# Performance work log

Measured on AMD Instinct MI355X. Metric: run time of the kernel, lower is better.

The kernel has to match this reference:

```python
import jax, jax.numpy as jnp
import numpy as np
import math

A, B, C = 32, 2048, 256   # batch, seq_len, features (M_size1)
TK, HA = 3, 8             # num_blocks, num_heads
DH = C // HA
EPS = 1e-5


def _layernorm(x, g, b):
    mu = jnp.mean(x, axis=-1, keepdims=True)
    var = jnp.mean((x - mu) ** 2, axis=-1, keepdims=True)
    return (x - mu) * jax.lax.rsqrt(var + EPS) * g + b


def setup_inputs() -> dict:
    key = jax.random.key(0)
    ks = jax.random.split(key, 12)
    # NOTE: torch code uses randn (std=1) for weight/Wqkv/Wo which explodes
    # numerically over 3 blocks + 2048-step cumsum; we use a small-std init
    # (like the trunc_normal(std=0.02) used for bias/cls) for a well-scaled
    # baseline. The math of the forward pass is unchanged.
    s = 0.02
    return {
        "x": jax.random.normal(ks[0], (A, B, C), jnp.float32),
        "weight": s * jax.random.normal(ks[1], (C, C), jnp.float32),
        "bias": s * jax.random.normal(ks[2], (A, B + 1, C), jnp.float32),
        "cls": s * jax.random.normal(ks[3], (A, 1, C), jnp.float32),
        "Wqkv": s * jax.random.normal(ks[4], (TK, 3, HA, DH, C), jnp.float32),
        "Wo": s * jax.random.normal(ks[5], (TK, C, C), jnp.float32),
        "ln1_g": jnp.ones((C,), jnp.float32),
        "ln1_b": jnp.zeros((C,), jnp.float32),
        "ln2_g": jnp.ones((C,), jnp.float32),
        "ln2_b": jnp.zeros((C,), jnp.float32),
        "fc1_w": s * jax.random.normal(ks[6], (4 * C, C), jnp.float32),
        "fc1_b": jnp.zeros((4 * C,), jnp.float32),
        "fc2_w": s * jax.random.normal(ks[7], (C, 4 * C), jnp.float32),
        "fc2_b": jnp.zeros((C,), jnp.float32),
    }


def reference(x, weight, bias, cls, Wqkv, Wo, ln1_g, ln1_b, ln2_g, ln2_b,
              fc1_w, fc1_b, fc2_w, fc2_b):
    # savespace[i,j,l] = sum_m weight[l,m] * x[i,j,m]   (torch: 'lm,jmi->ijl')
    savespace = jnp.einsum('ijm,lm->ijl', x, weight)              # (A,B,C)
    savespace = jnp.concatenate([cls, savespace], axis=1) + bias  # (A,B+1,C)

    inv_sqrt_dh = 1.0 / math.sqrt(DH)
    for a in range(TK):
        z = _layernorm(savespace, ln1_g, ln1_b)
        # (3,HA,DH,C) x (A,B+1,C) -> (3,A,B+1,HA,DH)
        qkv = jnp.einsum('xhdm,ijm->xijhd', Wqkv[a], z)
        q, k, v = qkv[0], qkv[1], qkv[2]
        rsa = jnp.sum(q * k, axis=-1) * inv_sqrt_dh               # (A,B+1,HA)
        imv = rsa[..., None] * v                                  # (A,B+1,HA,DH)
        # torch loop: subj in range(1, B) -> cumsum over positions 0..B-1,
        # last position (index B) left untouched.
        imv = jnp.concatenate(
            [jnp.cumsum(imv[:, :B], axis=1), imv[:, B:]], axis=1)
        imv = imv.reshape(A, B + 1, C)
        savespace = jnp.einsum('nm,ijm->ijn', Wo[a], imv) + savespace
        z2 = _layernorm(savespace, ln2_g, ln2_b)
        h = jax.nn.gelu(z2 @ fc1_w.T + fc1_b, approximate=False)
        savespace = h @ fc2_w.T + fc2_b + savespace
    return savespace
```

## Files before the change

### kernel.cpp

```cpp
#include <hip/hip_runtime.h>
#include <math.h>

#define AA 32
#define BB 2048
#define BP1 2049
#define CC 256
#define NROWS (AA * BP1)
#define NBLK 3
#define FFN 1024

typedef unsigned int uint;
typedef unsigned short ushort_t;
typedef __attribute__((ext_vector_type(4))) float f32x4;
typedef __attribute__((ext_vector_type(8))) short short8;

#define F_ROWMAP 2
#define F_BIAS2D 4
#define F_BIAS1D 8
#define F_GELU   16
#define F_RESID  32
#define F_OUTB16 64
#define F_QKV    128

__device__ __forceinline__ float bf2f(ushort_t u) {
    return __uint_as_float(((uint)u) << 16);
}
__device__ __forceinline__ ushort_t f2b(float x) {
    uint u = __float_as_uint(x);
    u += 0x7fff + ((u >> 16) & 1);
    return (ushort_t)(u >> 16);
}

typedef const uint __attribute__((address_space(1)))* gas_t;
typedef uint __attribute__((address_space(3)))* las_t;
__device__ __forceinline__ void gload16(const ushort_t* g, const short* l) {
    __builtin_amdgcn_global_load_lds(
        reinterpret_cast<gas_t>(reinterpret_cast<uintptr_t>(g)),
        reinterpret_cast<las_t>(static_cast<uint>(reinterpret_cast<uintptr_t>(l))),
        16, 0, 0);
}

__global__ __launch_bounds__(256) void pack2_k(const float* __restrict__ src,
                                               ushort_t* __restrict__ dh,
                                               ushort_t* __restrict__ dl, int n) {
    int i = blockIdx.x * 256 + threadIdx.x;
    if (i < n) {
        float v = src[i];
        ushort_t h = f2b(v);
        dh[i] = h;
        if (dl) dl[i] = f2b(v - bf2f(h));
    }
}

__global__ __launch_bounds__(256) void wqkv_pack_k(const float* __restrict__ src,
                                                   ushort_t* __restrict__ dh,
                                                   ushort_t* __restrict__ dl) {
    int i = blockIdx.x * 256 + threadIdx.x;
    if (i >= 589824) return;
    int c = i & 255;
    int rr = (i >> 8) % 768;
    int a = i / (768 * 256);
    int srcrow;
    if (rr < 512) {
        int head = rr >> 6, half = (rr >> 5) & 1, d = rr & 31;
        srcrow = half * 256 + head * 32 + d;
    } else {
        srcrow = rr;
    }
    float v = src[((size_t)a * 768 + srcrow) * 256 + c];
    ushort_t h = f2b(v);
    dh[i] = h;
    dl[i] = f2b(v - bf2f(h));
}

__global__ __launch_bounds__(256) void row0_k(float* __restrict__ out,
                                              const float* __restrict__ cls,
                                              const float* __restrict__ bias) {
    int i = blockIdx.x, t = threadIdx.x;
    size_t o = (size_t)i * BP1 * CC + t;
    out[o] = cls[i * CC + t] + bias[o];
}

__global__ __launch_bounds__(256) void ln_k(const float* __restrict__ in,
                                            ushort_t* __restrict__ zh, ushort_t* __restrict__ zl,
                                            const float* __restrict__ g, const float* __restrict__ b) {
    int row = blockIdx.x * 4 + (threadIdx.x >> 6);
    int lane = threadIdx.x & 63;
    const float4 v = *reinterpret_cast<const float4*>(in + (size_t)row * CC + lane * 4);
    float s = v.x + v.y + v.z + v.w;
    float sq = v.x * v.x + v.y * v.y + v.z * v.z + v.w * v.w;
    #pragma unroll
    for (int m = 1; m < 64; m <<= 1) { s += __shfl_xor(s, m); sq += __shfl_xor(sq, m); }
    float mu = s * (1.0f / CC);
    float var = sq * (1.0f / CC) - mu * mu;
    float rs = rsqrtf(var + 1e-5f);
    const float4 gg = *reinterpret_cast<const float4*>(g + lane * 4);
    const float4 bb = *reinterpret_cast<const float4*>(b + lane * 4);
    float o[4];
    o[0] = (v.x - mu) * rs * gg.x + bb.x;
    o[1] = (v.y - mu) * rs * gg.y + bb.y;
    o[2] = (v.z - mu) * rs * gg.z + bb.z;
    o[3] = (v.w - mu) * rs * gg.w + bb.w;
    ushort4 hs;
    hs.x = f2b(o[0]); hs.y = f2b(o[1]); hs.z = f2b(o[2]); hs.w = f2b(o[3]);
    size_t base = (size_t)row * CC + lane * 4;
    *reinterpret_cast<ushort4*>(zh + base) = hs;
    if (zl) {
        ushort4 ls;
        ls.x = f2b(o[0] - bf2f(hs.x));
        ls.y = f2b(o[1] - bf2f(hs.y));
        ls.z = f2b(o[2] - bf2f(hs.z));
        ls.w = f2b(o[3] - bf2f(hs.w));
        *reinterpret_cast<ushort4*>(zl + base) = ls;
    }
}

__global__ __launch_bounds__(256) void cumsum1_k(const ushort_t* __restrict__ v,
                                                 const float* __restrict__ rsa,
                                                 float* __restrict__ tot) {
    int bi = blockIdx.x >> 5, ch = blockIdx.x & 31, c = threadIdx.x;
    int h = c >> 5;
    size_t row0 = (size_t)bi * BP1 + ch * 64;
    float s = 0.f;
    for (int j = 0; j < 64; ++j)
        s += bf2f(v[(row0 + j) * CC + c]) * rsa[(row0 + j) * 8 + h];
    tot[((size_t)bi * 32 + ch) * CC + c] = s;
}

__global__ __launch_bounds__(256) void cumsum2_k(const ushort_t* __restrict__ v,
                                                 const float* __restrict__ rsa,
                                                 const float* __restrict__ tot,
                                                 ushort_t* __restrict__ ph) {
    int bi = blockIdx.x / 33, ch = blockIdx.x - bi * 33, c = threadIdx.x;
    int h = c >> 5;
    if (ch == 32) {
        size_t row = (size_t)bi * BP1 + BB;
        float val = bf2f(v[row * CC + c]) * rsa[row * 8 + h];
        ph[row * CC + c] = f2b(val);
        return;
    }
    float s = 0.f;
    for (int q = 0; q < ch; ++q) s += tot[((size_t)bi * 32 + q) * CC + c];
    size_t row0 = (size_t)bi * BP1 + ch * 64;
    for (int j = 0; j < 64; ++j) {
        size_t row = row0 + j;
        s += bf2f(v[row * CC + c]) * rsa[row * 8 + h];
        ph[row * CC + c] = f2b(s);
    }
}

template<int ALO, int WLO>
__global__ __launch_bounds__(64) void mm_k(const ushort_t* __restrict__ Ah_g,
                                           const ushort_t* __restrict__ Al_g,
                                           const ushort_t* __restrict__ Bh_g,
                                           const ushort_t* __restrict__ Bl_g,
                                           void* __restrict__ Op,
                                           void* __restrict__ Op2,
                                           const float* __restrict__ bias,
                                           int M, int K, int NC, int NT, int flags) {
    __shared__ __align__(16) short As_h[2048];
    __shared__ __align__(16) short As_l[ALO ? 2048 : 8];
    __shared__ __align__(16) short Bs_h[2048];
    __shared__ __align__(16) short Bs_l[WLO ? 2048 : 8];
    const int l = threadIdx.x;

    const int nwg = gridDim.x;
    const int q8 = nwg >> 3, r8 = nwg & 7;
    const int xcd = blockIdx.x & 7, ii = blockIdx.x >> 3;
    const int wgid = (xcd < r8 ? xcd * (q8 + 1) : r8 * (q8 + 1) + (xcd - r8) * q8) + ii;
    const int nt = wgid % NT, mt = wgid / NT;
    const int n0 = nt * 64, m0 = mt * 64;

    const int sc = (l & 3) * 8;
    const int lr = l >> 2;
    size_t aoff[4], boff[4];
    #pragma unroll
    for (int c = 0; c < 4; ++c) {
        int ra = m0 + c * 16 + lr; if (ra >= M) ra = M - 1;
        aoff[c] = (size_t)ra * K + sc;
        boff[c] = (size_t)(n0 + c * 16 + lr) * K + sc;
    }

    f32x4 acc[4][4];
    #pragma unroll
    for (int i = 0; i < 4; ++i)
        #pragma unroll
        for (int j = 0; j < 4; ++j) acc[i][j] = (f32x4)(0.0f);

    for (int k0 = 0; k0 < K; k0 += 32) {
        #pragma unroll
        for (int c = 0; c < 4; ++c) {
            gload16(Ah_g + aoff[c] + k0, &As_h[c * 512]);
            if (ALO) gload16(Al_g + aoff[c] + k0, &As_l[c * 512]);
            gload16(Bh_g + boff[c] + k0, &Bs_h[c * 512]);
            if (WLO) gload16(Bl_g + boff[c] + k0, &Bs_l[c * 512]);
        }
        asm volatile("s_waitcnt vmcnt(0)" ::: "memory");
        __builtin_amdgcn_sched_barrier(0);
        short8 ah[4], al[4], bh[4], bl[4];
        #pragma unroll
        for (int i = 0; i < 4; ++i) {
            int ro = (i * 16 + (l & 15)) * 32 + (l >> 4) * 8;
            ah[i] = *reinterpret_cast<const short8*>(&As_h[ro]);
            if (ALO) al[i] = *reinterpret_cast<const short8*>(&As_l[ro]);
        }
        #pragma unroll
        for (int j = 0; j < 4; ++j) {
            int ro = (j * 16 + (l & 15)) * 32 + (l >> 4) * 8;
            bh[j] = *reinterpret_cast<const short8*>(&Bs_h[ro]);
            if (WLO) bl[j] = *reinterpret_cast<const short8*>(&Bs_l[ro]);
        }
        #pragma unroll
        for (int i = 0; i < 4; ++i)
            #pragma unroll
            for (int j = 0; j < 4; ++j) {
                acc[i][j] = __builtin_amdgcn_mfma_f32_16x16x32_bf16(bh[j], ah[i], acc[i][j], 0, 0, 0);
                if (WLO)
                    acc[i][j] = __builtin_amdgcn_mfma_f32_16x16x32_bf16(bl[j], ah[i], acc[i][j], 0, 0, 0);
                if (ALO)
                    acc[i][j] = __builtin_amdgcn_mfma_f32_16x16x32_bf16(bh[j], al[i], acc[i][j], 0, 0, 0);
            }
        __builtin_amdgcn_sched_barrier(0);
    }

    if (flags & F_QKV) {
        const int cb0 = n0;
        if (cb0 < 512) {
            float* rsaO = reinterpret_cast<float*>(Op);
            const int head = cb0 >> 6;
            #pragma unroll
            for (int i = 0; i < 4; ++i) {
                int row = m0 + i * 16 + (l & 15);
                float p = 0.f;
                #pragma unroll
                for (int j = 0; j < 2; ++j)
                    #pragma unroll
                    for (int r = 0; r < 4; ++r)
                        p += acc[i][j][r] * acc[i][j + 2][r];
                p += __shfl_xor(p, 16);
                p += __shfl_xor(p, 32);
                if (l < 16 && row < M)
                    rsaO[(size_t)row * 8 + head] = p * 0.17677669529663689f;
            }
        } else {
            ushort_t* vO = reinterpret_cast<ushort_t*>(Op2);
            #pragma unroll
            for (int i = 0; i < 4; ++i) {
                int row = m0 + i * 16 + (l & 15);
                if (row >= M) continue;
                #pragma unroll
                for (int j = 0; j < 4; ++j) {
                    int colb = cb0 + j * 16 + (l >> 4) * 4 - 512;
                    uint2 u;
                    u.x = (uint)f2b(acc[i][j][0]) | ((uint)f2b(acc[i][j][1]) << 16);
                    u.y = (uint)f2b(acc[i][j][2]) | ((uint)f2b(acc[i][j][3]) << 16);
                    *reinterpret_cast<uint2*>(vO + (size_t)row * 256 + colb) = u;
                }
            }
        }
        return;
    }

    #pragma unroll
    for (int i = 0; i < 4; ++i) {
        int row = m0 + i * 16 + (l & 15);
        if (row >= M) continue;
        size_t g = (flags & F_ROWMAP) ? ((size_t)(row >> 11) * BP1 + 1 + (row & 2047))
                                     : (size_t)row;
        #pragma unroll
        for (int j = 0; j < 4; ++j) {
            int col0 = n0 + j * 16 + (l >> 4) * 4;
            float4 v4 = make_float4(acc[i][j][0], acc[i][j][1], acc[i][j][2], acc[i][j][3]);
            if (flags & F_BIAS1D) {
                const float4 b4 = *reinterpret_cast<const float4*>(bias + col0);
                v4.x += b4.x; v4.y += b4.y; v4.z += b4.z; v4.w += b4.w;
            }
            if (flags & F_BIAS2D) {
                const float4 b4 = *reinterpret_cast<const float4*>(bias + g * (size_t)NC + col0);
                v4.x += b4.x; v4.y += b4.y; v4.z += b4.z; v4.w += b4.w;
            }
            if (flags & F_GELU) {
                float z0 = v4.x * (1.595769122f + 0.071354816f * v4.x * v4.x);
                float z1 = v4.y * (1.595769122f + 0.071354816f * v4.y * v4.y);
                float z2 = v4.z * (1.595769122f + 0.071354816f * v4.z * v4.z);
                float z3 = v4.w * (1.595769122f + 0.071354816f * v4.w * v4.w);
                v4.x = v4.x / (1.0f + __expf(-z0));
                v4.y = v4.y / (1.0f + __expf(-z1));
                v4.z = v4.z / (1.0f + __expf(-z2));
                v4.w = v4.w / (1.0f + __expf(-z3));
            }
            size_t oi = g * (size_t)NC + col0;
            if (flags & F_OUTB16) {
                uint2 u;
                u.x = (uint)f2b(v4.x) | ((uint)f2b(v4.y) << 16);
                u.y = (uint)f2b(v4.z) | ((uint)f2b(v4.w) << 16);
                *reinterpret_cast<uint2*>(reinterpret_cast<ushort_t*>(Op) + oi) = u;
            } else {
                float* O = reinterpret_cast<float*>(Op) + oi;
                if (flags & F_RESID) {
                    const float4 o4 = *reinterpret_cast<const float4*>(O);
                    v4.x += o4.x; v4.y += o4.y; v4.z += o4.z; v4.w += o4.w;
                }
                *reinterpret_cast<float4*>(O) = v4;
            }
        }
    }
}

extern "C" void kernel_launch(void* const* d_in, const int* in_sizes, int n_in,
                              void* d_out, int out_size, void* d_ws, size_t ws_size,
                              hipStream_t stream) {
    const float* x      = (const float*)d_in[0];
    const float* weight = (const float*)d_in[1];
    const float* bias   = (const float*)d_in[2];
    const float* cls    = (const float*)d_in[3];
    const float* Wqkv   = (const float*)d_in[4];
    const float* Wo     = (const float*)d_in[5];
    const float* ln1_g  = (const float*)d_in[6];
    const float* ln1_b  = (const float*)d_in[7];
    const float* ln2_g  = (const float*)d_in[8];
    const float* ln2_b  = (const float*)d_in[9];
    const float* fc1_w  = (const float*)d_in[10];
    const float* fc1_b  = (const float*)d_in[11];
    const float* fc2_w  = (const float*)d_in[12];
    const float* fc2_b  = (const float*)d_in[13];
    float* out = (float*)d_out;

    char* ws = (char*)d_ws;
    ushort_t* zh    = (ushort_t*)(ws + 0);
    float*    tot   = (float*)(ws + 33570816);
    ushort_t* vbuf  = (ushort_t*)(ws + 67141632);
    ushort_t* imh   = (ushort_t*)(ws + 134283264);
    ushort_t* hbuf  = (ushort_t*)(ws + 67141632);
    float*    rsa   = (float*)(ws + 201424896);
    ushort_t* wp    = (ushort_t*)(ws + 203785216);

    ushort_t* w_h    = wp;
    ushort_t* w_l    = wp + 65536;
    ushort_t* wqkv_h = wp + 131072;
    ushort_t* wqkv_l = wp + 720896;
    ushort_t* wo_h   = wp + 1310720;
    ushort_t* wo_l   = wp + 1507328;
    ushort_t* fc1_h  = wp + 1703936;
    ushort_t* fc2_h  = wp + 2228224;
    ushort_t* fc2_l  = wp + 2490368;

    pack2_k<<<256,  256, 0, stream>>>(weight, w_h,    w_l,    65536);
    wqkv_pack_k<<<2304, 256, 0, stream>>>(Wqkv, wqkv_h, wqkv_l);
    pack2_k<<<768,  256, 0, stream>>>(Wo,     wo_h,   wo_l,   196608);
    pack2_k<<<1024, 256, 0, stream>>>(fc1_w,  fc1_h,  nullptr, 262144);
    pack2_k<<<1024, 256, 0, stream>>>(fc2_w,  fc2_h,  fc2_l,  262144);
    pack2_k<<<65536, 256, 0, stream>>>(x, zh, nullptr, AA * BB * CC);

    row0_k<<<AA, 256, 0, stream>>>(out, cls, bias);
    mm_k<0,1><<<4 * 1024, 64, 0, stream>>>(zh, nullptr, w_h, w_l, out, nullptr, bias,
                                           AA * BB, CC, CC, 4, F_ROWMAP | F_BIAS2D);

    const int MT = (NROWS + 63) / 64;
    for (int a = 0; a < NBLK; ++a) {
        const size_t aw = (size_t)a * 196608;
        ln_k<<<NROWS / 4, 256, 0, stream>>>(out, zh, nullptr, ln1_g, ln1_b);
        mm_k<0,1><<<12 * MT, 64, 0, stream>>>(zh, nullptr, wqkv_h + aw, wqkv_l + aw,
                                              rsa, vbuf, nullptr,
                                              NROWS, CC, 768, 12, F_QKV);
        cumsum1_k<<<1024, 256, 0, stream>>>(vbuf, rsa, tot);
        cumsum2_k<<<1056, 256, 0, stream>>>(vbuf, rsa, tot, imh);
        mm_k<0,1><<<4 * MT, 64, 0, stream>>>(imh, nullptr, wo_h + (size_t)a * 65536,
                                             wo_l + (size_t)a * 65536, out, nullptr, nullptr,
                                             NROWS, CC, CC, 4, F_RESID);
        ln_k<<<NROWS / 4, 256, 0, stream>>>(out, zh, nullptr, ln2_g, ln2_b);
        mm_k<0,0><<<16 * MT, 64, 0, stream>>>(zh, nullptr, fc1_h, nullptr, hbuf, nullptr, fc1_b,
                                              NROWS, CC, FFN, 16, F_BIAS1D | F_GELU | F_OUTB16);
        mm_k<0,1><<<4 * MT, 64, 0, stream>>>(hbuf, nullptr, fc2_h, fc2_l, out, nullptr, fc2_b,
                                             NROWS, FFN, CC, 4, F_BIAS1D | F_RESID);
    }
}
```

Measured before the change: 1.310 ms.

## Double-buffer LDS tiles in GEMM kernel to overlap global loads with MFMA

Doubles the shared-memory A/B tile buffers and prefetches the next K-tile while the current tile is being consumed. A partial vmcnt wait holds back only the just-issued loads, so global-to-LDS latency can overlap with the MFMA work. This doubles LDS use per workgroup, which can reduce occupancy. It also relies on the vmcnt count matching the number of loads issued per stage, and on a single wave per block so that no barrier is needed before the other buffer is overwritten.

```diff
diff --git a/kernel.cpp b/kernel.cpp
--- a/kernel.cpp
+++ b/kernel.cpp
@@ -158,11 +158,12 @@
                                            void* __restrict__ Op2,
                                            const float* __restrict__ bias,
                                            int M, int K, int NC, int NT, int flags) {
-    __shared__ __align__(16) short As_h[2048];
-    __shared__ __align__(16) short As_l[ALO ? 2048 : 8];
-    __shared__ __align__(16) short Bs_h[2048];
-    __shared__ __align__(16) short Bs_l[WLO ? 2048 : 8];
+    __shared__ __align__(16) short As_h[2][2048];
+    __shared__ __align__(16) short As_l[ALO ? 2 : 1][ALO ? 2048 : 8];
+    __shared__ __align__(16) short Bs_h[2][2048];
+    __shared__ __align__(16) short Bs_l[WLO ? 2 : 1][WLO ? 2048 : 8];
     const int l = threadIdx.x;
+    constexpr int LPS = 4 * (1 + ALO) + 4 * (1 + WLO);
 
     const int nwg = gridDim.x;
     const int q8 = nwg >> 3, r8 = nwg & 7;
@@ -187,28 +188,42 @@
         #pragma unroll
         for (int j = 0; j < 4; ++j) acc[i][j] = (f32x4)(0.0f);
 
-    for (int k0 = 0; k0 < K; k0 += 32) {
-        #pragma unroll
-        for (int c = 0; c < 4; ++c) {
-            gload16(Ah_g + aoff[c] + k0, &As_h[c * 512]);
-            if (ALO) gload16(Al_g + aoff[c] + k0, &As_l[c * 512]);
-            gload16(Bh_g + boff[c] + k0, &Bs_h[c * 512]);
-            if (WLO) gload16(Bl_g + boff[c] + k0, &Bs_l[c * 512]);
-        }
-        asm volatile("s_waitcnt vmcnt(0)" ::: "memory");
+    #define STAGE(buf, kk)                                                    \
+        do {                                                                  \
+            _Pragma("unroll")                                                 \
+            for (int c = 0; c < 4; ++c) {                                     \
+                gload16(Ah_g + aoff[c] + (kk), &As_h[buf][c * 512]);          \
+                if (ALO) gload16(Al_g + aoff[c] + (kk), &As_l[buf][c * 512]); \
+                gload16(Bh_g + boff[c] + (kk), &Bs_h[buf][c * 512]);          \
+                if (WLO) gload16(Bl_g + boff[c] + (kk), &Bs_l[buf][c * 512]); \
+            }                                                                 \
+        } while (0)
+
+    const int ntile = K >> 5;
+    STAGE(0, 0);
+    for (int tt = 0; tt < ntile; ++tt) {
+        const int cur = tt & 1;
+        if (tt + 1 < ntile) {
+            STAGE(cur ^ 1, (tt + 1) * 32);
+            if constexpr (LPS == 8)       asm volatile("s_waitcnt vmcnt(8)"  ::: "memory");
+            else if constexpr (LPS == 12) asm volatile("s_waitcnt vmcnt(12)" ::: "memory");
+            else                          asm volatile("s_waitcnt vmcnt(16)" ::: "memory");
+        } else {
+            asm volatile("s_waitcnt vmcnt(0)" ::: "memory");
+        }
         __builtin_amdgcn_sched_barrier(0);
         short8 ah[4], al[4], bh[4], bl[4];
         #pragma unroll
         for (int i = 0; i < 4; ++i) {
             int ro = (i * 16 + (l & 15)) * 32 + (l >> 4) * 8;
-            ah[i] = *reinterpret_cast<const short8*>(&As_h[ro]);
-            if (ALO) al[i] = *reinterpret_cast<const short8*>(&As_l[ro]);
+            ah[i] = *reinterpret_cast<const short8*>(&As_h[cur][ro]);
+            if (ALO) al[i] = *reinterpret_cast<const short8*>(&As_l[cur][ro]);
         }
         #pragma unroll
         for (int j = 0; j < 4; ++j) {
             int ro = (j * 16 + (l & 15)) * 32 + (l >> 4) * 8;
-            bh[j] = *reinterpret_cast<const short8*>(&Bs_h[ro]);
-            if (WLO) bl[j] = *reinterpret_cast<const short8*>(&Bs_l[ro]);
+            bh[j] = *reinterpret_cast<const short8*>(&Bs_h[cur][ro]);
+            if (WLO) bl[j] = *reinterpret_cast<const short8*>(&Bs_l[cur][ro]);
         }
         #pragma unroll
         for (int i = 0; i < 4; ++i)
@@ -222,6 +237,7 @@
             }
         __builtin_amdgcn_sched_barrier(0);
     }
+    #undef STAGE
 
     if (flags & F_QKV) {
         const int cb0 = n0;
```

Result: no change. 1.329 ms (+1.4%).
